# Kernel tuning notes

Hardware: AMD Instinct MI355X
Metric: run time of the kernel (lower is better)

## Reference

```python
import jax, jax.numpy as jnp
import numpy as np

N = 20000        # nodes
E = 640000       # edges (avg degree 32)
D_IN = 128       # node_features
D_HID = 256      # conv_booster * D_IN
D_DENSE = 128    # D_HID // linear_decay
N_CLASSES = 2


def _glorot(key, fan_in, fan_out):
    s = np.sqrt(1.0 / fan_in).astype(np.float32)
    return jax.random.normal(key, (fan_in, fan_out), jnp.float32) * s


def setup_inputs() -> dict:
    key = jax.random.key(0)
    ks = jax.random.split(key, 12)
    return {
        "node_features": jax.random.normal(ks[0], (N, D_IN), jnp.float32),
        "edge_index": jax.random.randint(ks[1], (2, E), 0, N, dtype=jnp.int32),
        "edge_weight": jax.random.uniform(ks[2], (E,), jnp.float32),
        "W1": _glorot(ks[3], D_IN, D_HID),
        "b1": jnp.zeros((D_HID,), jnp.float32),
        "W2": _glorot(ks[4], D_HID, D_HID),
        "b2": jnp.zeros((D_HID,), jnp.float32),
        "Wd1": _glorot(ks[5], D_HID, D_DENSE),
        "bd1": jnp.zeros((D_DENSE,), jnp.float32),
        "Wd2": _glorot(ks[6], D_DENSE, N_CLASSES),
        "bd2": jnp.zeros((N_CLASSES,), jnp.float32),
    }


def gcn_conv(x, row, col, w, W, b, n):
    # PyG GCNConv: add self-loops (weight 1), symmetric normalization,
    # x' = D^{-1/2}(A+I)D^{-1/2} (x W) + b
    h = x @ W                                        # [n, out]
    loop = jnp.arange(n, dtype=row.dtype)
    r = jnp.concatenate([row, loop])
    c = jnp.concatenate([col, loop])
    ww = jnp.concatenate([w, jnp.ones((n,), w.dtype)])
    deg = jax.ops.segment_sum(ww, c, num_segments=n)  # degree at targets
    dinv = jnp.where(deg > 0, jax.lax.rsqrt(deg), 0.0)
    norm = dinv[r] * ww * dinv[c]                    # [E+n]
    msg = norm[:, None] * h[r]                       # gather + scale (hot path)
    return jax.ops.segment_sum(msg, c, num_segments=n) + b  # scatter-add


def reference(node_features, edge_index, edge_weight,
              W1, b1, W2, b2, Wd1, bd1, Wd2, bd2):
    row, col = edge_index[0], edge_index[1]
    n = node_features.shape[0]
    h = gcn_conv(node_features, row, col, edge_weight, W1, b1, n)
    h = gcn_conv(h, row, col, edge_weight, W2, b2, n)
    g = jnp.mean(h, axis=0)                          # MeanAggregation pooling
    z = jax.nn.relu(g @ Wd1 + bd1)
    logits = z @ Wd2 + bd2
    return jax.nn.softmax(logits)
```

## Files before the change

kernel.cpp:

```cpp
#include <hip/hip_runtime.h>
#include <hip/hip_bf16.h>


#define D_IN 128
#define D_HID 256
#define D_DENSE 128
#define R0 10240
#define NSL 64
#define NFOLD 79

__global__ __launch_bounds__(1024) void k_scatter(
    const int* __restrict__ tgt, const int* __restrict__ src,
    const float* __restrict__ w, const float* __restrict__ dinv,
    const float* __restrict__ u, float* __restrict__ part,
    int E, int N, int mode) {
    __shared__ float acc[R0];
    const int range = blockIdx.x & 1;
    const int slice = blockIdx.x >> 1;
    const int base  = range ? R0 : 0;
    const int lim   = range ? (N - R0) : R0;
    if (lim <= 0) return;
    const int per = (E + NSL - 1) / NSL;
    const int e0 = slice * per, e1 = min(e0 + per, E);
    float* outp = part + (range ? (size_t)NSL * R0 + (size_t)slice * lim
                                : (size_t)slice * lim);
    for (int i = threadIdx.x; i < lim; i += 1024) acc[i] = 0.f;
    __syncthreads();
    for (int e = e0 + threadIdx.x; e < e1; e += 1024) {
        int t = tgt[e] - base;
        if ((unsigned)t < (unsigned)lim) {
            float v = w[e];
            if (mode != 0) {
                int c = src[e];
                float dc = dinv[c];
                v *= (mode == 2) ? dc * u[c] : dc;
            }
            atomicAdd(&acc[t], v);
        }
    }
    __syncthreads();
    for (int i = threadIdx.x; i < lim; i += 1024) outp[i] = acc[i];
}

__global__ __launch_bounds__(1024) void k_fold(
    const float* __restrict__ part, float* __restrict__ dinv,
    float* __restrict__ u, float* __restrict__ wv,
    float* __restrict__ S_u_part,
    const float* __restrict__ W1, const float* __restrict__ b1,
    const float* __restrict__ W2, float* __restrict__ M, float* __restrict__ c2,
    int N, int mode) {
    __shared__ float lds[1056];
    const int b = blockIdx.x, tid = threadIdx.x;

    if (b >= NFOLD) {
        int q = b - NFOLD;
        lds[tid] = W2[(tid >> 2) * 256 + q * 4 + (tid & 3)];
        __syncthreads();
        int wvi = tid >> 6, lane = tid & 63;
        for (int kr = 0; kr < 8; ++kr) {
            int k = wvi * 8 + kr;
            float a0 = 0, a1 = 0, a2 = 0, a3 = 0;
            #pragma unroll
            for (int it = 0; it < 4; ++it) {
                int j = it * 64 + lane;
                float a = W1[k * 256 + j];
                a0 += a * lds[j*4+0]; a1 += a * lds[j*4+1];
                a2 += a * lds[j*4+2]; a3 += a * lds[j*4+3];
            }
            #pragma unroll
            for (int off = 32; off > 0; off >>= 1) {
                a0 += __shfl_down(a0, off, 64); a1 += __shfl_down(a1, off, 64);
                a2 += __shfl_down(a2, off, 64); a3 += __shfl_down(a3, off, 64);
            }
            if (lane == 0) {
                M[k * 256 + q*4 + 0] = a0; M[k * 256 + q*4 + 1] = a1;
                M[k * 256 + q*4 + 2] = a2; M[k * 256 + q*4 + 3] = a3;
            }
        }
        if (wvi == 0) {
            float a0 = 0, a1 = 0, a2 = 0, a3 = 0;
            #pragma unroll
            for (int it = 0; it < 4; ++it) {
                int j = it * 64 + lane;
                float a = b1[j];
                a0 += a * lds[j*4+0]; a1 += a * lds[j*4+1];
                a2 += a * lds[j*4+2]; a3 += a * lds[j*4+3];
            }
            #pragma unroll
            for (int off = 32; off > 0; off >>= 1) {
                a0 += __shfl_down(a0, off, 64); a1 += __shfl_down(a1, off, 64);
                a2 += __shfl_down(a2, off, 64); a3 += __shfl_down(a3, off, 64);
            }
            if (lane == 0) {
                c2[q*4+0] = a0; c2[q*4+1] = a1;
                c2[q*4+2] = a2; c2[q*4+3] = a3;
            }
        }
        return;
    }

    const int j = tid & 255, rg = tid >> 8;
    const int i = b * 256 + j;
    const bool act = i < N;
    const int R1 = N - R0;
    float sv = 0.f;
    if (act) {
        const float* pp;
        size_t st;
        if (i < R0) { pp = part + i;                          st = R0; }
        else        { pp = part + (size_t)NSL * R0 + (i - R0); st = R1; }
        pp += (size_t)rg * 16 * st;
        #pragma unroll
        for (int r = 0; r < 16; ++r) sv += pp[(size_t)r * st];
    }
    lds[rg * 256 + j] = sv;
    __syncthreads();
    float ui = 0.f;
    if (rg == 0) {
        float tot = lds[j] + lds[256 + j] + lds[512 + j] + lds[768 + j];
        if (act) {
            if (mode == 0)      dinv[i] = rsqrtf(tot + 1.0f);
            else if (mode == 1) { float d = dinv[i]; ui = d * (tot + d); u[i] = ui; }
            else                { float d = dinv[i]; wv[i] = d * (tot + d * u[i]); }
        }
    }
    if (mode == 1) {
        float v = ui;
        #pragma unroll
        for (int off = 32; off > 0; off >>= 1) v += __shfl_down(v, off, 64);
        if (tid < 256 && (tid & 63) == 0) lds[1024 + (tid >> 6)] = v;
        __syncthreads();
        if (tid == 0)
            S_u_part[b] = lds[1024] + lds[1025] + lds[1026] + lds[1027];
    }
}

__device__ __forceinline__ void g_arrive(unsigned* ctr) {
    __syncthreads();
    if (threadIdx.x == 0)
        __hip_atomic_fetch_add(ctr, 1u, __ATOMIC_RELEASE, __HIP_MEMORY_SCOPE_AGENT);
}
__device__ __forceinline__ void g_wait(unsigned* ctr, unsigned target) {
    if (threadIdx.x == 0) {
        while (__hip_atomic_load(ctr, __ATOMIC_ACQUIRE, __HIP_MEMORY_SCOPE_AGENT) < target)
            __builtin_amdgcn_s_sleep(2);
    }
    __syncthreads();
}

__global__ __launch_bounds__(256) void k_tail(
    const float* __restrict__ x, const float* __restrict__ wv,
    const float* __restrict__ S_u_part, const float* __restrict__ M,
    const float* __restrict__ c2, const float* __restrict__ b2,
    const float* __restrict__ Wd1, const float* __restrict__ bd1,
    const float* __restrict__ Wd2, const float* __restrict__ bd2,
    float* __restrict__ s_part, float* __restrict__ g_part,
    float* __restrict__ z_part, float* __restrict__ S_u_g,
    unsigned* __restrict__ ctr, float* __restrict__ out,
    int N, float inv_n) {
    __shared__ float sh[256];
    __shared__ float ss[128];
    __shared__ float gv[16];
    const int b = blockIdx.x, tid = threadIdx.x;
    const int k = tid & 127, h = tid >> 7;

    float acc = 0.f;
    for (int i = b * 2 + h; i < N; i += 512)
        acc += wv[i] * x[(size_t)i * D_IN + k];
    sh[h * 128 + k] = acc;
    __syncthreads();
    if (h == 0) s_part[b * 128 + k] = sh[k] + sh[128 + k];
    g_arrive(ctr);
    if (b >= 16) return;
    g_wait(ctr, 256);

    {
        float a2 = 0.f;
        for (int q = 0; q < 128; ++q)
            a2 += s_part[(h * 128 + q) * 128 + k];
        sh[h * 128 + k] = a2;
        __syncthreads();
        if (h == 0) ss[k] = sh[k] + sh[128 + k];
        if (b == 0) {
            float v = (tid < NFOLD) ? S_u_part[tid] : 0.f;
            #pragma unroll
            for (int off = 32; off > 0; off >>= 1) v += __shfl_down(v, off, 64);
            if ((tid & 63) == 0) sh[(tid >> 6)] = v;
        }
        __syncthreads();
        if (b == 0 && tid == 0)
            S_u_g[0] = sh[0] + sh[1] + sh[2] + sh[3];
        float gp = 0.f;
        #pragma unroll
        for (int kk = 0; kk < 8; ++kk)
            gp += ss[b * 8 + kk] * M[(b * 8 + kk) * 256 + tid];
        g_part[b * 256 + tid] = gp;
    }
    g_arrive(ctr);
    g_wait(ctr, 272);

    {
        if (tid < 16) {
            int kk = b * 16 + tid;
            float gval = 0.f;
            #pragma unroll
            for (int p2 = 0; p2 < 16; ++p2) gval += g_part[p2 * 256 + kk];
            gv[tid] = (gval + S_u_g[0] * c2[kk]) * inv_n + b2[kk];
        }
        __syncthreads();
        if (tid < 128) {
            float z = 0.f;
            #pragma unroll
            for (int kk = 0; kk < 16; ++kk)
                z += gv[kk] * Wd1[(b * 16 + kk) * D_DENSE + tid];
            z_part[b * 128 + tid] = z;
        }
    }
    g_arrive(ctr);
    if (b != 0) return;
    g_wait(ctr, 288);

    float p0 = 0.f, p1 = 0.f;
    if (tid < 128) {
        float zr = bd1[tid];
        #pragma unroll
        for (int p2 = 0; p2 < 16; ++p2) zr += z_part[p2 * 128 + tid];
        float zt = fmaxf(zr, 0.f);
        p0 = zt * Wd2[tid * 2 + 0];
        p1 = zt * Wd2[tid * 2 + 1];
    }
    #pragma unroll
    for (int off = 32; off > 0; off >>= 1) {
        p0 += __shfl_down(p0, off, 64);
        p1 += __shfl_down(p1, off, 64);
    }
    if ((tid & 63) == 0) { sh[tid >> 6] = p0; sh[16 + (tid >> 6)] = p1; }
    __syncthreads();
    if (tid == 0) {
        float l0 = sh[0] + sh[1] + sh[2] + sh[3] + bd2[0];
        float l1 = sh[16] + sh[17] + sh[18] + sh[19] + bd2[1];
        float m = fmaxf(l0, l1);
        float e0 = expf(l0 - m), e1 = expf(l1 - m);
        float inv = 1.0f / (e0 + e1);
        out[0] = e0 * inv;
        out[1] = e1 * inv;
    }
}

extern "C" void kernel_launch(void* const* d_in, const int* in_sizes, int n_in,
                              void* d_out, int out_size, void* d_ws, size_t ws_size,
                              hipStream_t stream) {
    const float* x   = (const float*)d_in[0];
    const int*   ei  = (const int*)  d_in[1];
    const float* w   = (const float*)d_in[2];
    const float* W1  = (const float*)d_in[3];
    const float* b1  = (const float*)d_in[4];
    const float* W2  = (const float*)d_in[5];
    const float* b2  = (const float*)d_in[6];
    const float* Wd1 = (const float*)d_in[7];
    const float* bd1 = (const float*)d_in[8];
    const float* Wd2 = (const float*)d_in[9];
    const float* bd2 = (const float*)d_in[10];
    float* out = (float*)d_out;

    const int N = in_sizes[0] / D_IN;
    const int E = in_sizes[1] / 2;
    const int* row = ei;
    const int* col = ei + E;

    float* ws     = (float*)d_ws;
    unsigned* ctr = (unsigned*)ws;
    float* part   = ws + 16;
    float* dinv   = part + (size_t)NSL * N;
    float* u      = dinv + N;
    float* wv     = u + N;
    float* s_part = wv + N;
    float* S_u_p  = s_part + 256 * D_IN;
    float* S_u_g  = S_u_p + 128;
    float* M      = S_u_g + 1;
    float* c2     = M + D_IN * D_HID;
    float* g_part = c2 + D_HID;
    float* z_part = g_part + 16 * D_HID;

    hipMemsetAsync(ctr, 0, 64, stream);

    k_scatter<<<2 * NSL, 1024, 0, stream>>>(col, row, w, dinv, u, part, E, N, 0);
    k_fold<<<NFOLD + 64, 1024, 0, stream>>>(part, dinv, u, wv, S_u_p,
                                            W1, b1, W2, M, c2, N, 0);
    k_scatter<<<2 * NSL, 1024, 0, stream>>>(row, col, w, dinv, u, part, E, N, 1);
    k_fold<<<NFOLD, 1024, 0, stream>>>(part, dinv, u, wv, S_u_p,
                                       W1, b1, W2, M, c2, N, 1);
    k_scatter<<<2 * NSL, 1024, 0, stream>>>(row, col, w, dinv, u, part, E, N, 2);
    k_fold<<<NFOLD, 1024, 0, stream>>>(part, dinv, u, wv, S_u_p,
                                       W1, b1, W2, M, c2, N, 2);
    k_tail<<<256, 256, 0, stream>>>(x, wv, S_u_p, M, c2, b2, Wd1, bd1, Wd2, bd2,
                                    s_part, g_part, z_part, S_u_g, ctr, out,
                                    N, 1.0f / (float)N);
}
```

Measured before the change: 161.0 us.

## Fuse final fold into tail kernel, double scatter slices, drop memset launch

The number of edge slices per scatter goes from 64 to 128, and the fold uses more, smaller blocks (80 nodes each, 250 blocks). The mode-2 fold kernel is removed. k_tail now reduces the scatter partials itself, computes the per-node weight in LDS, and does the weighted sum over x directly, which removes a launch and the wv round-trip through global memory. The host memset of the grid counter is replaced by a reset inside the first scatter kernel. In exchange, the partial buffer doubles, so the fold and tail read more data, and each tail block performs a 128-deep strided reduction.

```diff
diff --git a/kernel.cpp b/kernel.cpp
--- a/kernel.cpp
+++ b/kernel.cpp
@@ -6,20 +6,22 @@
 #define D_HID 256
 #define D_DENSE 128
 #define R0 10240
-#define NSL 64
-#define NFOLD 79
+#define NSL 128
+#define NFOLD 250
+#define FOLD_C 80
+#define NTILE 157
 
 __global__ __launch_bounds__(1024) void k_scatter(
     const int* __restrict__ tgt, const int* __restrict__ src,
     const float* __restrict__ w, const float* __restrict__ dinv,
     const float* __restrict__ u, float* __restrict__ part,
-    int E, int N, int mode) {
+    unsigned* __restrict__ ctr, int E, int N, int mode) {
     __shared__ float acc[R0];
+    if (mode == 0 && blockIdx.x == 0 && threadIdx.x == 0) ctr[0] = 0u;
     const int range = blockIdx.x & 1;
     const int slice = blockIdx.x >> 1;
     const int base  = range ? R0 : 0;
     const int lim   = range ? (N - R0) : R0;
-    if (lim <= 0) return;
     const int per = (E + NSL - 1) / NSL;
     const int e0 = slice * per, e1 = min(e0 + per, E);
     float* outp = part + (range ? (size_t)NSL * R0 + (size_t)slice * lim
@@ -44,12 +46,11 @@
 
 __global__ __launch_bounds__(1024) void k_fold(
     const float* __restrict__ part, float* __restrict__ dinv,
-    float* __restrict__ u, float* __restrict__ wv,
-    float* __restrict__ S_u_part,
+    float* __restrict__ u, float* __restrict__ S_u_part,
     const float* __restrict__ W1, const float* __restrict__ b1,
     const float* __restrict__ W2, float* __restrict__ M, float* __restrict__ c2,
     int N, int mode) {
-    __shared__ float lds[1056];
+    __shared__ float lds[1044];
     const int b = blockIdx.x, tid = threadIdx.x;
 
     if (b >= NFOLD) {
@@ -99,39 +100,42 @@
         return;
     }
 
-    const int j = tid & 255, rg = tid >> 8;
-    const int i = b * 256 + j;
-    const bool act = i < N;
-    const int R1 = N - R0;
+    const int j = tid & 127, rg = tid >> 7;
+    const int i = b * FOLD_C + j;
+    const bool act = (j < FOLD_C) && (i < N);
     float sv = 0.f;
     if (act) {
-        const float* pp;
-        size_t st;
-        if (i < R0) { pp = part + i;                          st = R0; }
-        else        { pp = part + (size_t)NSL * R0 + (i - R0); st = R1; }
+        size_t st; const float* pp;
+        if (i < R0) { st = R0;            pp = part + i; }
+        else        { st = (size_t)(N - R0); pp = part + (size_t)NSL * R0 + (i - R0); }
         pp += (size_t)rg * 16 * st;
         #pragma unroll
         for (int r = 0; r < 16; ++r) sv += pp[(size_t)r * st];
     }
-    lds[rg * 256 + j] = sv;
+    lds[rg * 128 + j] = sv;
     __syncthreads();
     float ui = 0.f;
     if (rg == 0) {
-        float tot = lds[j] + lds[256 + j] + lds[512 + j] + lds[768 + j];
+        float tot = 0.f;
+        #pragma unroll
+        for (int q = 0; q < 8; ++q) tot += lds[q * 128 + j];
         if (act) {
-            if (mode == 0)      dinv[i] = rsqrtf(tot + 1.0f);
-            else if (mode == 1) { float d = dinv[i]; ui = d * (tot + d); u[i] = ui; }
-            else                { float d = dinv[i]; wv[i] = d * (tot + d * u[i]); }
+            if (mode == 0) dinv[i] = rsqrtf(tot + 1.0f);
+            else { float d = dinv[i]; ui = d * (tot + d); u[i] = ui; }
         }
     }
     if (mode == 1) {
         float v = ui;
         #pragma unroll
         for (int off = 32; off > 0; off >>= 1) v += __shfl_down(v, off, 64);
-        if (tid < 256 && (tid & 63) == 0) lds[1024 + (tid >> 6)] = v;
-        __syncthreads();
-        if (tid == 0)
-            S_u_part[b] = lds[1024] + lds[1025] + lds[1026] + lds[1027];
+        if ((tid & 63) == 0) lds[1028 + (tid >> 6)] = v;
+        __syncthreads();
+        if (tid == 0) {
+            float t2 = 0.f;
+            #pragma unroll
+            for (int q = 0; q < 16; ++q) t2 += lds[1028 + q];
+            S_u_part[b] = t2;
+        }
     }
 }
 
@@ -149,7 +153,8 @@
 }
 
 __global__ __launch_bounds__(256) void k_tail(
-    const float* __restrict__ x, const float* __restrict__ wv,
+    const float* __restrict__ x, const float* __restrict__ part,
+    const float* __restrict__ dinv, const float* __restrict__ u,
     const float* __restrict__ S_u_part, const float* __restrict__ M,
     const float* __restrict__ c2, const float* __restrict__ b2,
     const float* __restrict__ Wd1, const float* __restrict__ bd1,
@@ -159,37 +164,63 @@
     unsigned* __restrict__ ctr, float* __restrict__ out,
     int N, float inv_n) {
     __shared__ float sh[256];
+    __shared__ float wvl[128];
     __shared__ float ss[128];
     __shared__ float gv[16];
+    __shared__ float su4[4];
     const int b = blockIdx.x, tid = threadIdx.x;
-    const int k = tid & 127, h = tid >> 7;
-
-    float acc = 0.f;
-    for (int i = b * 2 + h; i < N; i += 512)
-        acc += wv[i] * x[(size_t)i * D_IN + k];
-    sh[h * 128 + k] = acc;
-    __syncthreads();
-    if (h == 0) s_part[b * 128 + k] = sh[k] + sh[128 + k];
+    const int k = tid & 127, rg = tid >> 7;
+
+    if (b < NTILE) {
+        const int i0 = b * 128;
+        const int i = i0 + k;
+        const bool act = i < N;
+        float sv = 0.f;
+        if (act) {
+            size_t st; const float* pp;
+            if (i < R0) { st = R0;               pp = part + i; }
+            else        { st = (size_t)(N - R0); pp = part + (size_t)NSL * R0 + (i - R0); }
+            pp += (size_t)rg * 64 * st;
+            #pragma unroll 16
+            for (int r = 0; r < 64; ++r) sv += pp[(size_t)r * st];
+        }
+        sh[tid] = sv;
+        __syncthreads();
+        if (rg == 0) {
+            float q = sh[k] + sh[128 + k];
+            float d = act ? dinv[i] : 0.f;
+            wvl[k] = act ? d * (q + d * u[i]) : 0.f;
+        }
+        __syncthreads();
+        float acc = 0.f;
+        for (int m = rg; m < 128; m += 2) {
+            int i2 = i0 + m;
+            if (i2 >= N) break;
+            acc += wvl[m] * x[(size_t)i2 * D_IN + k];
+        }
+        sh[tid] = acc;
+        __syncthreads();
+        if (rg == 0) s_part[b * 128 + k] = sh[k] + sh[128 + k];
+    }
     g_arrive(ctr);
     if (b >= 16) return;
     g_wait(ctr, 256);
 
     {
         float a2 = 0.f;
-        for (int q = 0; q < 128; ++q)
-            a2 += s_part[(h * 128 + q) * 128 + k];
-        sh[h * 128 + k] = a2;
-        __syncthreads();
-        if (h == 0) ss[k] = sh[k] + sh[128 + k];
+        for (int q = rg; q < NTILE; q += 2) a2 += s_part[q * 128 + k];
+        sh[tid] = a2;
+        float v = 0.f;
         if (b == 0) {
-            float v = (tid < NFOLD) ? S_u_part[tid] : 0.f;
+            v = (tid < NFOLD) ? S_u_part[tid] : 0.f;
             #pragma unroll
             for (int off = 32; off > 0; off >>= 1) v += __shfl_down(v, off, 64);
-            if ((tid & 63) == 0) sh[(tid >> 6)] = v;
-        }
-        __syncthreads();
-        if (b == 0 && tid == 0)
-            S_u_g[0] = sh[0] + sh[1] + sh[2] + sh[3];
+        }
+        __syncthreads();
+        if (rg == 0) ss[k] = sh[k] + sh[128 + k];
+        if (b == 0 && (tid & 63) == 0) su4[tid >> 6] = v;
+        __syncthreads();
+        if (b == 0 && tid == 0) S_u_g[0] = su4[0] + su4[1] + su4[2] + su4[3];
         float gp = 0.f;
         #pragma unroll
         for (int kk = 0; kk < 8; ++kk)
@@ -268,32 +299,25 @@
     const int* row = ei;
     const int* col = ei + E;
 
-    float* ws     = (float*)d_ws;
-    unsigned* ctr = (unsigned*)ws;
-    float* part   = ws + 16;
+    unsigned* ctr = (unsigned*)d_ws;
+    float* fws    = (float*)d_ws + 16;
+    float* part   = fws;
     float* dinv   = part + (size_t)NSL * N;
     float* u      = dinv + N;
-    float* wv     = u + N;
-    float* s_part = wv + N;
-    float* S_u_p  = s_part + 256 * D_IN;
-    float* S_u_g  = S_u_p + 128;
+    float* s_part = u + N;
+    float* S_u_p  = s_part + (size_t)NTILE * D_IN;
+    float* S_u_g  = S_u_p + NFOLD;
     float* M      = S_u_g + 1;
     float* c2     = M + D_IN * D_HID;
     float* g_part = c2 + D_HID;
     float* z_part = g_part + 16 * D_HID;
 
-    hipMemsetAsync(ctr, 0, 64, stream);
-
-    k_scatter<<<2 * NSL, 1024, 0, stream>>>(col, row, w, dinv, u, part, E, N, 0);
-    k_fold<<<NFOLD + 64, 1024, 0, stream>>>(part, dinv, u, wv, S_u_p,
-                                            W1, b1, W2, M, c2, N, 0);
-    k_scatter<<<2 * NSL, 1024, 0, stream>>>(row, col, w, dinv, u, part, E, N, 1);
-    k_fold<<<NFOLD, 1024, 0, stream>>>(part, dinv, u, wv, S_u_p,
-                                       W1, b1, W2, M, c2, N, 1);
-    k_scatter<<<2 * NSL, 1024, 0, stream>>>(row, col, w, dinv, u, part, E, N, 2);
-    k_fold<<<NFOLD, 1024, 0, stream>>>(part, dinv, u, wv, S_u_p,
-                                       W1, b1, W2, M, c2, N, 2);
-    k_tail<<<256, 256, 0, stream>>>(x, wv, S_u_p, M, c2, b2, Wd1, bd1, Wd2, bd2,
-                                    s_part, g_part, z_part, S_u_g, ctr, out,
-                                    N, 1.0f / (float)N);
-}
+    k_scatter<<<2 * NSL, 1024, 0, stream>>>(col, row, w, dinv, u, part, ctr, E, N, 0);
+    k_fold<<<NFOLD + 64, 1024, 0, stream>>>(part, dinv, u, S_u_p, W1, b1, W2, M, c2, N, 0);
+    k_scatter<<<2 * NSL, 1024, 0, stream>>>(row, col, w, dinv, u, part, ctr, E, N, 1);
+    k_fold<<<NFOLD, 1024, 0, stream>>>(part, dinv, u, S_u_p, W1, b1, W2, M, c2, N, 1);
+    k_scatter<<<2 * NSL, 1024, 0, stream>>>(row, col, w, dinv, u, part, ctr, E, N, 2);
+    k_tail<<<256, 256, 0, stream>>>(x, part, dinv, u, S_u_p, M, c2, b2,
+                                    Wd1, bd1, Wd2, bd2, s_part, g_part, z_part,
+                                    S_u_g, ctr, out, N, 1.0f / (float)N);
+}
```

Result: slower. 177.9 us (+10.5%).
